# Performance work log

Hardware: AMD Instinct MI355X
Metric: run time of the kernel (lower is better)

Reference implementation:

```python
import jax, jax.numpy as jnp
from jax import lax
import numpy as np

KSIZE = 3        # patch-matching kernel
RATE = 2         # dilation/upsample rate
FUSE_K = 3       # fusion kernel size
SCALE = 10.0     # softmax scale
EPS = 1e-4


def _same_pads(size, k, s):
    # TF 'SAME' padding: total pad so out = ceil(size / s)
    out = -(-size // s)
    total = max(0, (out - 1) * s + k - size)
    top = total // 2
    return (top, total - top)


def _extract_patches(x, k, s):
    # x: [N,C,H,W] -> [N, L, C, k, k], SAME padding, row-major patch order
    ph = _same_pads(x.shape[2], k, s)
    pw = _same_pads(x.shape[3], k, s)
    p = lax.conv_general_dilated_patches(x, (k, k), (s, s), (ph, pw))
    N, _, Ho, Wo = p.shape
    C = x.shape[1]
    p = p.reshape(N, C, k, k, Ho * Wo)  # channel-major patch layout (matches torch unfold)
    return jnp.transpose(p, (0, 4, 1, 2, 3))


def setup_inputs() -> dict:
    key = jax.random.key(0)
    k1, k2 = jax.random.split(key)
    f = jax.random.normal(k1, (8, 96, 64, 64), dtype=jnp.float32)
    b = jax.random.normal(k2, (8, 96, 64, 64), dtype=jnp.float32)
    return {"f": f, "b": b}


def reference(f, b):
    # TF-style nearest-neighbor downsample (stride sampling)
    fs = f[:, :, ::RATE, ::RATE]
    bs = b[:, :, ::RATE, ::RATE]
    N, C, H, W = fs.shape  # downsampled dims; f and b share shape here
    L = H * W
    kernel = 2 * RATE

    # raw background patches for aggregation: [N, L, C, 2r, 2r]
    raw_w = _extract_patches(b, kernel, RATE)
    # matching patches from downsampled background: [N, L, C, 3, 3]
    w = _extract_patches(bs, KSIZE, 1)

    fuse_w = jnp.eye(FUSE_K, dtype=f.dtype).reshape(1, 1, FUSE_K, FUSE_K)
    ct_pad = kernel - 1 - 1  # conv_transpose padding=1 -> conv pad k-1-p = 2

    def attend(xi, wi, rwi):
        # xi: [C,H,W]; wi: [L,C,3,3]; rwi: [L,C,2r,2r]
        norm = jnp.sqrt(jnp.sum(wi * wi, axis=(1, 2, 3), keepdims=True))
        wn = wi / jnp.maximum(norm, EPS)
        # cosine-similarity correlation: [L,H,W]
        yi = lax.conv_general_dilated(xi[None], wn, (1, 1), ((1, 1), (1, 1)))[0]
        # fusion: identity-kernel convs over the [L_b, L_f] score map, both orientations
        y2 = yi.reshape(1, 1, L, L)
        y2 = lax.conv_general_dilated(y2, fuse_w, (1, 1), ((1, 1), (1, 1)))
        y2 = jnp.transpose(y2.reshape(H, W, H, W), (1, 0, 3, 2)).reshape(1, 1, L, L)
        y2 = lax.conv_general_dilated(y2, fuse_w, (1, 1), ((1, 1), (1, 1)))
        yi = jnp.transpose(y2.reshape(W, H, W, H), (1, 0, 3, 2)).reshape(L, H, W)
        # softmax over background patches (mask mm == 1 since mask is None)
        yi = jax.nn.softmax(yi * SCALE, axis=0)
        # conv_transpose2d(yi, rwi, stride=RATE, padding=1) / 4
        wct = jnp.flip(jnp.swapaxes(rwi, 0, 1), axis=(2, 3))  # [C, L, 2r, 2r]
        out = lax.conv_general_dilated(
            yi[None], wct, (1, 1), ((ct_pad, ct_pad), (ct_pad, ct_pad)),
            lhs_dilation=(RATE, RATE))[0]
        return out / 4.0

    y = jax.vmap(attend)(fs, w, raw_w)  # [N, C, H*RATE, W*RATE]
    return y.reshape(f.shape)
```

## Files before the change

kernel.cpp:

```cpp
#include <hip/hip_runtime.h>
#include <math.h>

#define NB 8
#define NC 96
#define HF 64
#define HS 32
#define L 1024
#define MN 1536

#define G_OFF    0ull
#define F1T_OFF  (8ull * 1024 * 1024)
#define YB_B     (64ull * 1024 * 1024)
#define RWT_B    (80ull * 1024 * 1024)
#define N_OFF    (27262976ull)
#define FS_OFF   (27271168ull)
#define BS_OFF   (28057600ull)
#define Z_OFF    0ull

typedef __attribute__((ext_vector_type(8))) short short8;
typedef __attribute__((ext_vector_type(4))) float float4v;

__device__ inline unsigned short f2bf(float x) {
    union { float f; unsigned u; } v; v.f = x;
    unsigned r = v.u + 0x7fff + ((v.u >> 16) & 1);
    return (unsigned short)(r >> 16);
}

__global__ void kpre_pack(const float* __restrict__ f, const float* __restrict__ b,
                          float* __restrict__ ws) {
    int n = blockIdx.x, c = blockIdx.y, which = blockIdx.z;
    const float* src = (which ? b : f) + ((size_t)n * NC + c) * (HF * HF);
    float* dst = ws + (which ? BS_OFF : FS_OFF) + ((size_t)n * NC + c) * 1024;
    int t = threadIdx.x;
    #pragma unroll
    for (int e = 0; e < 4; ++e) {
        int pos = t + e * 256;
        int i = pos >> 5, j = pos & 31;
        dst[pos] = src[(2 * i) * HF + 2 * j];
    }
}

__global__ void k0_norm(float* __restrict__ ws) {
    int n = blockIdx.x;
    int t = threadIdx.x;
    int i = t >> 5, j = t & 31;
    __shared__ float sq[1024];
    const float* bsp = ws + BS_OFF + (size_t)n * NC * 1024;
    float s = 0.f;
    for (int c = 0; c < NC; ++c) {
        float v = bsp[(size_t)c * 1024 + t];
        s += v * v;
    }
    sq[t] = s;
    __syncthreads();
    float nsq = 0.f;
    #pragma unroll
    for (int dy = -1; dy <= 1; ++dy)
        #pragma unroll
        for (int dx = -1; dx <= 1; ++dx) {
            int ii = i + dy, jj = j + dx;
            if (ii >= 0 && ii < HS && jj >= 0 && jj < HS) nsq += sq[ii * HS + jj];
        }
    ws[N_OFF + (size_t)n * L + t] = 1.f / fmaxf(sqrtf(nsq), 1e-4f);
}

__global__ __launch_bounds__(256) void k1_gram(float* __restrict__ ws) {
    int n = blockIdx.x;
    int p0 = blockIdx.y * 128, l0 = blockIdx.z * 128;
    int t = threadIdx.x;
    int tp = t >> 4, tm = t & 15;
    __shared__ float Bt[32][132];
    __shared__ float Ft[32][132];
    float acc[8][8] = {};
    const float* bsp = ws + BS_OFF + (size_t)n * NC * 1024;
    const float* fsp = ws + FS_OFF + (size_t)n * NC * 1024;
    for (int c0 = 0; c0 < NC; c0 += 32) {
        #pragma unroll
        for (int e = 0; e < 4; ++e) {
            int idx = t + e * 256;
            int cl = idx >> 5, vq = idx & 31;
            *(float4*)&Bt[cl][vq * 4] =
                *(const float4*)&bsp[(size_t)(c0 + cl) * 1024 + l0 + vq * 4];
            *(float4*)&Ft[cl][vq * 4] =
                *(const float4*)&fsp[(size_t)(c0 + cl) * 1024 + p0 + vq * 4];
        }
        __syncthreads();
        for (int cl = 0; cl < 32; ++cl) {
            float4 a0 = *(const float4*)&Bt[cl][tp * 8];
            float4 a1 = *(const float4*)&Bt[cl][tp * 8 + 4];
            float4 b0 = *(const float4*)&Ft[cl][tm * 8];
            float4 b1 = *(const float4*)&Ft[cl][tm * 8 + 4];
            float av[8] = {a0.x, a0.y, a0.z, a0.w, a1.x, a1.y, a1.z, a1.w};
            float bv[8] = {b0.x, b0.y, b0.z, b0.w, b1.x, b1.y, b1.z, b1.w};
            #pragma unroll
            for (int aa = 0; aa < 8; ++aa)
                #pragma unroll
                for (int bb = 0; bb < 8; ++bb)
                    acc[aa][bb] += av[aa] * bv[bb];
        }
        __syncthreads();
    }
    float* G = ws + G_OFF + (size_t)n * L * L;
    #pragma unroll
    for (int aa = 0; aa < 8; ++aa) {
        int l = l0 + tp * 8 + aa;
        *(float4*)&G[(size_t)l * L + p0 + tm * 8] =
            make_float4(acc[aa][0], acc[aa][1], acc[aa][2], acc[aa][3]);
        *(float4*)&G[(size_t)l * L + p0 + tm * 8 + 4] =
            make_float4(acc[aa][4], acc[aa][5], acc[aa][6], acc[aa][7]);
    }
}

__global__ __launch_bounds__(256) void k23_score_fuse1t(float* __restrict__ ws) {
    int bid = blockIdx.x;
    int n = bid & 7;
    int tile = bid >> 3;
    int i0 = (tile >> 5) * 32, j0 = (tile & 31) * 32;
    int t = threadIdx.x;
    __shared__ float U[36][37];
    __shared__ float sA[34][35];
    __shared__ float sinv[34];
    const float* G = ws + G_OFF + (size_t)n * L * L;
    const float* invn = ws + N_OFF + (size_t)n * L;
    if (t < 34) {
        int l = i0 - 1 + t;
        sinv[t] = ((unsigned)l < L) ? invn[l] : 0.f;
    }
    for (int e = 0; e < 6; ++e) {
        int idx = t + e * 256;
        if (idx < 1296) {
            int a = idx / 36, bq = idx - a * 36;
            int l = i0 - 2 + a, p = j0 - 2 + bq;
            float s = 0.f;
            #pragma unroll
            for (int dy = -1; dy <= 1; ++dy) {
                int ll = l + dy * 32, pp = p + dy * 32;
                if ((unsigned)ll < L && (unsigned)pp < L)
                    s += G[(size_t)ll * L + pp];
            }
            U[a][bq] = s;
        }
    }
    __syncthreads();
    for (int e = 0; e < 5; ++e) {
        int idx = t + e * 256;
        if (idx < 1156) {
            int ih = idx / 34, jh = idx - ih * 34;
            int l = i0 - 1 + ih, p = j0 - 1 + jh;
            float a = 0.f;
            if ((unsigned)l < L && (unsigned)p < L) {
                int lx = l & 31, px = p & 31;
                float s = 0.f;
                #pragma unroll
                for (int dx = -1; dx <= 1; ++dx) {
                    bool ok = (unsigned)(lx + dx) < HS && (unsigned)(px + dx) < HS;
                    float u = U[ih + 1 + dx][jh + 1 + dx];
                    s += ok ? u : 0.f;
                }
                a = sinv[ih] * s;
            }
            sA[ih][jh] = a;
        }
    }
    __syncthreads();
    float* F1T = ws + F1T_OFF + (size_t)n * L * L;
    #pragma unroll
    for (int e = 0; e < 4; ++e) {
        int idx = t + e * 256;
        int jl = idx >> 5, il = idx & 31;
        float v = sA[il][jl] + sA[il + 1][jl + 1] + sA[il + 2][jl + 2];
        F1T[(size_t)(j0 + jl) * L + i0 + il] = v;
    }
}

__global__ void k4_fuse2_softmax(float* __restrict__ ws) {
    int bid = blockIdx.x;
    int n = bid & 7, p = bid >> 3;
    int t = threadIdx.x;
    int py = p >> 5, px = p & 31;
    int Jc = px * HS + py;
    __shared__ float s3[3][32][33];
    __shared__ float red[8];
    const float* F1T = ws + F1T_OFF + (size_t)n * L * L;
    #pragma unroll
    for (int d = 0; d < 3; ++d) {
        int Jd = Jc + d - 1;
        bool ok = (Jd >= 0 && Jd < L);
        int rd = ok ? ((Jd & 31) * HS + (Jd >> 5)) : 0;
        const float* row = F1T + (size_t)rd * L;
        for (int e = 0; e < 4; ++e) {
            int i_ = t + e * 256;
            float v = ok ? row[i_] : 0.f;
            s3[d][i_ & 31][i_ >> 5] = v;
        }
    }
    __syncthreads();
    float vals[4];
    float mymax = -1e30f;
    #pragma unroll
    for (int e = 0; e < 4; ++e) {
        int kk = t + e * 256;
        float v = 0.f;
        #pragma unroll
        for (int d = 0; d < 3; ++d) {
            int kd = kk + d - 1;
            if (kd >= 0 && kd < L) v += s3[d][kd >> 5][kd & 31];
        }
        v *= 10.0f;
        vals[e] = v;
        mymax = fmaxf(mymax, v);
    }
    #pragma unroll
    for (int off = 32; off > 0; off >>= 1)
        mymax = fmaxf(mymax, __shfl_xor(mymax, off));
    if ((t & 63) == 0) red[t >> 6] = mymax;
    __syncthreads();
    float Mx = fmaxf(fmaxf(red[0], red[1]), fmaxf(red[2], red[3]));
    float mysum = 0.f;
    #pragma unroll
    for (int e = 0; e < 4; ++e) { vals[e] = __expf(vals[e] - Mx); mysum += vals[e]; }
    #pragma unroll
    for (int off = 32; off > 0; off >>= 1)
        mysum += __shfl_xor(mysum, off);
    if ((t & 63) == 0) red[4 + (t >> 6)] = mysum;
    __syncthreads();
    float rinv = 1.f / (red[4] + red[5] + red[6] + red[7]);
    unsigned short* YbF = (unsigned short*)((char*)ws + YB_B) + (size_t)n * L * L;
    int pt = p >> 4, fr = p & 15;
    #pragma unroll
    for (int e = 0; e < 4; ++e) {
        int kk = t + e * 256;
        int kc = kk >> 5, qd = (kk >> 3) & 3, j = kk & 7;
        YbF[((size_t)pt * 32 + kc) * 512 + (qd * 16 + fr) * 8 + j] = f2bf(vals[e] * rinv);
    }
}

__global__ void k5_rwt(const float* __restrict__ b, float* __restrict__ ws) {
    int n = blockIdx.x, c = blockIdx.y;
    int t = threadIdx.x;
    __shared__ float pl[64][65];
    const float* bp = b + ((size_t)n * NC + c) * (HF * HF);
    for (int e = 0; e < 16; ++e) {
        int idx = t + e * 256;
        pl[idx >> 6][idx & 63] = bp[idx];
    }
    __syncthreads();
    unsigned short* RWtF = (unsigned short*)((char*)ws + RWT_B) + (size_t)n * MN * L
                           + (size_t)c * 32 * 512;
    #pragma unroll
    for (int uv = 0; uv < 16; ++uv) {
        int u = uv >> 2, v = uv & 3;
        for (int e = 0; e < 4; ++e) {
            int k = t + e * 256;
            int ly = k & 31, lx = k >> 5;
            int r = 2 * ly - 1 + u, s = 2 * lx - 1 + v;
            float val = (r >= 0 && r < HF && s >= 0 && s < HF) ? pl[r][s] : 0.f;
            int kc = k >> 5, qd = (k >> 3) & 3, j = k & 7;
            RWtF[(size_t)kc * 512 + (qd * 16 + uv) * 8 + j] = f2bf(val);
        }
    }
}

__global__ __launch_bounds__(256) void k6_mfma_z(float* __restrict__ ws) {
    int n = blockIdx.x;
    int wv = threadIdx.x >> 6, lane = threadIdx.x & 63;
    int pt0 = blockIdx.z * 8 + (wv >> 1) * 4;
    int mt0 = blockIdx.y * 8 + (wv & 1) * 4;

    const unsigned short* YbF = (const unsigned short*)((const char*)ws + YB_B)
                                + (size_t)n * L * L + lane * 8;
    const unsigned short* RWtF = (const unsigned short*)((const char*)ws + RWT_B)
                                 + (size_t)n * MN * L + lane * 8;

    float4v acc[4][4] = {};
    short8 af[2][4], bf[2][4];
    #pragma unroll
    for (int a = 0; a < 4; ++a) {
        af[0][a] = *(const short8*)(YbF + ((size_t)(pt0 + a) * 32) * 512);
        bf[0][a] = *(const short8*)(RWtF + ((size_t)(mt0 + a) * 32) * 512);
    }
    for (int kc = 0; kc < 32; ++kc) {
        int cur = kc & 1, nxt = cur ^ 1;
        if (kc < 31) {
            #pragma unroll
            for (int a = 0; a < 4; ++a) {
                af[nxt][a] = *(const short8*)(YbF + ((size_t)(pt0 + a) * 32 + kc + 1) * 512);
                bf[nxt][a] = *(const short8*)(RWtF + ((size_t)(mt0 + a) * 32 + kc + 1) * 512);
            }
        }
        #pragma unroll
        for (int a = 0; a < 4; ++a)
            #pragma unroll
            for (int bq = 0; bq < 4; ++bq)
                acc[a][bq] = __builtin_amdgcn_mfma_f32_16x16x32_bf16(
                    af[cur][a], bf[cur][bq], acc[a][bq], 0, 0, 0);
    }

    int fr = lane & 15, qd = lane >> 4;
    float* Zp = ws + Z_OFF + (size_t)n * L * MN;
    #pragma unroll
    for (int a = 0; a < 4; ++a) {
        #pragma unroll
        for (int r = 0; r < 4; ++r) {
            int p = (pt0 + a) * 16 + qd * 4 + r;
            #pragma unroll
            for (int bq = 0; bq < 4; ++bq) {
                int m = (mt0 + bq) * 16 + fr;
                Zp[(size_t)p * MN + m] = acc[a][bq][r];
            }
        }
    }
}

__global__ __launch_bounds__(256) void k7_gather(const float* __restrict__ ws,
                                                 float* __restrict__ out) {
    int n = blockIdx.x, yq = blockIdx.y, c = blockIdx.z;
    int t = threadIdx.x;
    int y0 = yq * 4;
    int ibase = (y0 >> 1) - 1;
    __shared__ float zs[128][17];
    const float* Zp = ws + Z_OFF + (size_t)n * L * MN;
    #pragma unroll
    for (int e = 0; e < 2; ++e) {
        int idx = t + e * 256;
        int pl = idx >> 2, q = idx & 3;
        int il = pl >> 5, j = pl & 31;
        int i = ibase + il;
        float4 v = make_float4(0.f, 0.f, 0.f, 0.f);
        if (i >= 0 && i < HS)
            v = *(const float4*)&Zp[(size_t)(i * HS + j) * MN + c * 16 + q * 4];
        zs[pl][q * 4 + 0] = v.x;
        zs[pl][q * 4 + 1] = v.y;
        zs[pl][q * 4 + 2] = v.z;
        zs[pl][q * 4 + 3] = v.w;
    }
    __syncthreads();
    int y = y0 + (t >> 6), x = t & 63;
    int ih = (y + 1) >> 1, jh = (x + 1) >> 1;
    float s = 0.f;
    #pragma unroll
    for (int di = 0; di < 2; ++di) {
        int i = ih - di;
        if (i < 0 || i >= HS) continue;
        int u = y + 1 - 2 * i;
        int il = i - ibase;
        #pragma unroll
        for (int dj = 0; dj < 2; ++dj) {
            int j = jh - dj;
            if (j < 0 || j >= HS) continue;
            int v = x + 1 - 2 * j;
            s += zs[il * 32 + j][u * 4 + v];
        }
    }
    out[(((size_t)n * NC + c) * HF + y) * HF + x] = 0.25f * s;
}

extern "C" void kernel_launch(void* const* d_in, const int* in_sizes, int n_in,
                              void* d_out, int out_size, void* d_ws, size_t ws_size,
                              hipStream_t stream) {
    const float* f = (const float*)d_in[0];
    const float* b = (const float*)d_in[1];
    float* out = (float*)d_out;
    float* ws = (float*)d_ws;

    kpre_pack<<<dim3(NB, NC, 2), 256, 0, stream>>>(f, b, ws);
    k0_norm<<<NB, 1024, 0, stream>>>(ws);
    k1_gram<<<dim3(NB, 8, 8), 256, 0, stream>>>(ws);
    k23_score_fuse1t<<<8192, 256, 0, stream>>>(ws);
    k4_fuse2_softmax<<<8192, 256, 0, stream>>>(ws);
    k5_rwt<<<dim3(NB, NC), 256, 0, stream>>>(b, ws);
    k6_mfma_z<<<dim3(NB, 12, 8), 256, 0, stream>>>(ws);
    k7_gather<<<dim3(NB, 16, NC), 256, 0, stream>>>(ws, out);
}
```

Baseline: 209.6 us.

## Fuse rwt into prep, share softmax rows across waves, store Z as bf16

```diff
diff --git a/kernel.cpp b/kernel.cpp
--- a/kernel.cpp
+++ b/kernel.cpp
@@ -15,7 +15,7 @@
 #define N_OFF    (27262976ull)
 #define FS_OFF   (27271168ull)
 #define BS_OFF   (28057600ull)
-#define Z_OFF    0ull
+#define ZB_B     0ull
 
 typedef __attribute__((ext_vector_type(8))) short short8;
 typedef __attribute__((ext_vector_type(4))) float float4v;
@@ -25,18 +25,53 @@
     unsigned r = v.u + 0x7fff + ((v.u >> 16) & 1);
     return (unsigned short)(r >> 16);
 }
-
-__global__ void kpre_pack(const float* __restrict__ f, const float* __restrict__ b,
-                          float* __restrict__ ws) {
-    int n = blockIdx.x, c = blockIdx.y, which = blockIdx.z;
-    const float* src = (which ? b : f) + ((size_t)n * NC + c) * (HF * HF);
-    float* dst = ws + (which ? BS_OFF : FS_OFF) + ((size_t)n * NC + c) * 1024;
-    int t = threadIdx.x;
+__device__ inline float bf2f(unsigned short h) {
+    union { unsigned u; float f; } v; v.u = ((unsigned)h) << 16;
+    return v.f;
+}
+
+__global__ void kprep(const float* __restrict__ f, const float* __restrict__ b,
+                      float* __restrict__ ws) {
+    int n = blockIdx.x, c = blockIdx.y, z = blockIdx.z;
+    int t = threadIdx.x;
+    if (z == 0) {
+        const float* src = f + ((size_t)n * NC + c) * (HF * HF);
+        float* dst = ws + FS_OFF + ((size_t)n * NC + c) * 1024;
+        #pragma unroll
+        for (int e = 0; e < 4; ++e) {
+            int pos = t + e * 256;
+            int i = pos >> 5, j = pos & 31;
+            dst[pos] = src[(2 * i) * HF + 2 * j];
+        }
+        return;
+    }
+    __shared__ float pl[64][65];
+    const float* bp = b + ((size_t)n * NC + c) * (HF * HF);
+    for (int e = 0; e < 16; ++e) {
+        int idx = t + e * 256;
+        pl[idx >> 6][idx & 63] = bp[idx];
+    }
+    __syncthreads();
+    float* bs = ws + BS_OFF + ((size_t)n * NC + c) * 1024;
     #pragma unroll
     for (int e = 0; e < 4; ++e) {
         int pos = t + e * 256;
         int i = pos >> 5, j = pos & 31;
-        dst[pos] = src[(2 * i) * HF + 2 * j];
+        bs[pos] = pl[2 * i][2 * j];
+    }
+    unsigned short* RWtF = (unsigned short*)((char*)ws + RWT_B) + (size_t)n * MN * L
+                           + (size_t)c * 32 * 512;
+    #pragma unroll
+    for (int uv = 0; uv < 16; ++uv) {
+        int u = uv >> 2, v = uv & 3;
+        for (int e = 0; e < 4; ++e) {
+            int k = t + e * 256;
+            int ly = k & 31, lx = k >> 5;
+            int r = 2 * ly - 1 + u, s = 2 * lx - 1 + v;
+            float val = (r >= 0 && r < HF && s >= 0 && s < HF) ? pl[r][s] : 0.f;
+            int kc = k >> 5, qd = (k >> 3) & 3, j = k & 7;
+            RWtF[(size_t)kc * 512 + (qd * 16 + uv) * 8 + j] = f2bf(val);
+        }
     }
 }
 
@@ -173,38 +208,42 @@
     }
 }
 
-__global__ void k4_fuse2_softmax(float* __restrict__ ws) {
-    int bid = blockIdx.x;
-    int n = bid & 7, p = bid >> 3;
-    int t = threadIdx.x;
-    int py = p >> 5, px = p & 31;
-    int Jc = px * HS + py;
-    __shared__ float s3[3][32][33];
-    __shared__ float red[8];
+__global__ __launch_bounds__(256) void k4_fuse2_softmax(float* __restrict__ ws) {
+    int n = blockIdx.x, px = blockIdx.y, py0 = blockIdx.z * 4;
+    int t = threadIdx.x;
+    __shared__ float trow[6][32][33];
     const float* F1T = ws + F1T_OFF + (size_t)n * L * L;
-    #pragma unroll
-    for (int d = 0; d < 3; ++d) {
-        int Jd = Jc + d - 1;
-        bool ok = (Jd >= 0 && Jd < L);
-        int rd = ok ? ((Jd & 31) * HS + (Jd >> 5)) : 0;
-        const float* row = F1T + (size_t)rd * L;
-        for (int e = 0; e < 4; ++e) {
-            int i_ = t + e * 256;
-            float v = ok ? row[i_] : 0.f;
-            s3[d][i_ & 31][i_ >> 5] = v;
-        }
-    }
-    __syncthreads();
-    float vals[4];
+    int Jbase = px * HS + py0;
+    #pragma unroll
+    for (int e = 0; e < 6; ++e) {
+        int idx = t + e * 256;
+        int d = idx >> 8, q = idx & 255;
+        int Jd = Jbase + d - 1;
+        float4 v = make_float4(0.f, 0.f, 0.f, 0.f);
+        if ((unsigned)Jd < L) {
+            int rd = (Jd & 31) * HS + (Jd >> 5);
+            v = *(const float4*)&F1T[(size_t)rd * L + 4 * q];
+        }
+        int col = q >> 3, r0 = (4 * q) & 31;
+        trow[d][r0 + 0][col] = v.x;
+        trow[d][r0 + 1][col] = v.y;
+        trow[d][r0 + 2][col] = v.z;
+        trow[d][r0 + 3][col] = v.w;
+    }
+    __syncthreads();
+    int w = t >> 6, ln = t & 63;
+    int py = py0 + w;
+    int p = py * HS + px;
+    float vals[16];
     float mymax = -1e30f;
     #pragma unroll
-    for (int e = 0; e < 4; ++e) {
-        int kk = t + e * 256;
+    for (int e = 0; e < 16; ++e) {
+        int k = e * 64 + ln;
         float v = 0.f;
         #pragma unroll
         for (int d = 0; d < 3; ++d) {
-            int kd = kk + d - 1;
-            if (kd >= 0 && kd < L) v += s3[d][kd >> 5][kd & 31];
+            int kd = k + d - 1;
+            if ((unsigned)kd < L) v += trow[w + d][kd >> 5][kd & 31];
         }
         v *= 10.0f;
         vals[e] = v;
@@ -213,51 +252,20 @@
     #pragma unroll
     for (int off = 32; off > 0; off >>= 1)
         mymax = fmaxf(mymax, __shfl_xor(mymax, off));
-    if ((t & 63) == 0) red[t >> 6] = mymax;
-    __syncthreads();
-    float Mx = fmaxf(fmaxf(red[0], red[1]), fmaxf(red[2], red[3]));
     float mysum = 0.f;
     #pragma unroll
-    for (int e = 0; e < 4; ++e) { vals[e] = __expf(vals[e] - Mx); mysum += vals[e]; }
+    for (int e = 0; e < 16; ++e) { vals[e] = __expf(vals[e] - mymax); mysum += vals[e]; }
     #pragma unroll
     for (int off = 32; off > 0; off >>= 1)
         mysum += __shfl_xor(mysum, off);
-    if ((t & 63) == 0) red[4 + (t >> 6)] = mysum;
-    __syncthreads();
-    float rinv = 1.f / (red[4] + red[5] + red[6] + red[7]);
+    float rinv = 1.f / mysum;
     unsigned short* YbF = (unsigned short*)((char*)ws + YB_B) + (size_t)n * L * L;
     int pt = p >> 4, fr = p & 15;
     #pragma unroll
-    for (int e = 0; e < 4; ++e) {
-        int kk = t + e * 256;
-        int kc = kk >> 5, qd = (kk >> 3) & 3, j = kk & 7;
+    for (int e = 0; e < 16; ++e) {
+        int k = e * 64 + ln;
+        int kc = k >> 5, qd = (k >> 3) & 3, j = k & 7;
         YbF[((size_t)pt * 32 + kc) * 512 + (qd * 16 + fr) * 8 + j] = f2bf(vals[e] * rinv);
-    }
-}
-
-__global__ void k5_rwt(const float* __restrict__ b, float* __restrict__ ws) {
-    int n = blockIdx.x, c = blockIdx.y;
-    int t = threadIdx.x;
-    __shared__ float pl[64][65];
-    const float* bp = b + ((size_t)n * NC + c) * (HF * HF);
-    for (int e = 0; e < 16; ++e) {
-        int idx = t + e * 256;
-        pl[idx >> 6][idx & 63] = bp[idx];
-    }
-    __syncthreads();
-    unsigned short* RWtF = (unsigned short*)((char*)ws + RWT_B) + (size_t)n * MN * L
-                           + (size_t)c * 32 * 512;
-    #pragma unroll
-    for (int uv = 0; uv < 16; ++uv) {
-        int u = uv >> 2, v = uv & 3;
-        for (int e = 0; e < 4; ++e) {
-            int k = t + e * 256;
-            int ly = k & 31, lx = k >> 5;
-            int r = 2 * ly - 1 + u, s = 2 * lx - 1 + v;
-            float val = (r >= 0 && r < HF && s >= 0 && s < HF) ? pl[r][s] : 0.f;
-            int kc = k >> 5, qd = (k >> 3) & 3, j = k & 7;
-            RWtF[(size_t)kc * 512 + (qd * 16 + uv) * 8 + j] = f2bf(val);
-        }
     }
 }
 
@@ -297,7 +305,7 @@
     }
 
     int fr = lane & 15, qd = lane >> 4;
-    float* Zp = ws + Z_OFF + (size_t)n * L * MN;
+    unsigned short* Zb = (unsigned short*)((char*)ws + ZB_B) + (size_t)n * L * MN;
     #pragma unroll
     for (int a = 0; a < 4; ++a) {
         #pragma unroll
@@ -306,7 +314,7 @@
             #pragma unroll
             for (int bq = 0; bq < 4; ++bq) {
                 int m = (mt0 + bq) * 16 + fr;
-                Zp[(size_t)p * MN + m] = acc[a][bq][r];
+                Zb[(size_t)p * MN + m] = f2bf(acc[a][bq][r]);
             }
         }
     }
@@ -314,30 +322,30 @@
 
 __global__ __launch_bounds__(256) void k7_gather(const float* __restrict__ ws,
                                                  float* __restrict__ out) {
-    int n = blockIdx.x, yq = blockIdx.y, c = blockIdx.z;
+    int n = blockIdx.x, yq = blockIdx.y, c0 = blockIdx.z * 2;
     int t = threadIdx.x;
     int y0 = yq * 4;
     int ibase = (y0 >> 1) - 1;
-    __shared__ float zs[128][17];
-    const float* Zp = ws + Z_OFF + (size_t)n * L * MN;
+    __shared__ float zs[128][33];
+    const unsigned short* Zb = (const unsigned short*)((const char*)ws + ZB_B)
+                               + (size_t)n * L * MN;
     #pragma unroll
     for (int e = 0; e < 2; ++e) {
         int idx = t + e * 256;
         int pl = idx >> 2, q = idx & 3;
         int il = pl >> 5, j = pl & 31;
         int i = ibase + il;
-        float4 v = make_float4(0.f, 0.f, 0.f, 0.f);
+        short8 v = {};
         if (i >= 0 && i < HS)
-            v = *(const float4*)&Zp[(size_t)(i * HS + j) * MN + c * 16 + q * 4];
-        zs[pl][q * 4 + 0] = v.x;
-        zs[pl][q * 4 + 1] = v.y;
-        zs[pl][q * 4 + 2] = v.z;
-        zs[pl][q * 4 + 3] = v.w;
+            v = *(const short8*)&Zb[(size_t)(i * HS + j) * MN + c0 * 16 + q * 8];
+        #pragma unroll
+        for (int m = 0; m < 8; ++m)
+            zs[pl][q * 8 + m] = bf2f((unsigned short)v[m]);
     }
     __syncthreads();
     int y = y0 + (t >> 6), x = t & 63;
     int ih = (y + 1) >> 1, jh = (x + 1) >> 1;
-    float s = 0.f;
+    float s0 = 0.f, s1 = 0.f;
     #pragma unroll
     for (int di = 0; di < 2; ++di) {
         int i = ih - di;
@@ -349,10 +357,12 @@
             int j = jh - dj;
             if (j < 0 || j >= HS) continue;
             int v = x + 1 - 2 * j;
-            s += zs[il * 32 + j][u * 4 + v];
-        }
-    }
-    out[(((size_t)n * NC + c) * HF + y) * HF + x] = 0.25f * s;
+            s0 += zs[il * 32 + j][u * 4 + v];
+            s1 += zs[il * 32 + j][16 + u * 4 + v];
+        }
+    }
+    out[(((size_t)n * NC + c0) * HF + y) * HF + x] = 0.25f * s0;
+    out[(((size_t)n * NC + c0 + 1) * HF + y) * HF + x] = 0.25f * s1;
 }
 
 extern "C" void kernel_launch(void* const* d_in, const int* in_sizes, int n_in,
@@ -363,12 +373,11 @@
     float* out = (float*)d_out;
     float* ws = (float*)d_ws;
 
-    kpre_pack<<<dim3(NB, NC, 2), 256, 0, stream>>>(f, b, ws);
+    kprep<<<dim3(NB, NC, 2), 256, 0, stream>>>(f, b, ws);
     k0_norm<<<NB, 1024, 0, stream>>>(ws);
     k1_gram<<<dim3(NB, 8, 8), 256, 0, stream>>>(ws);
     k23_score_fuse1t<<<8192, 256, 0, stream>>>(ws);
-    k4_fuse2_softmax<<<8192, 256, 0, stream>>>(ws);
-    k5_rwt<<<dim3(NB, NC), 256, 0, stream>>>(b, ws);
+    k4_fuse2_softmax<<<dim3(NB, 32, 8), 256, 0, stream>>>(ws);
     k6_mfma_z<<<dim3(NB, 12, 8), 256, 0, stream>>>(ws);
-    k7_gather<<<dim3(NB, 16, NC), 256, 0, stream>>>(ws, out);
-}
+    k7_gather<<<dim3(NB, 16, 48), 256, 0, stream>>>(ws, out);
+}
```

After: 233.0 us. 1.11x slower.
